# Kernel optimization log

Hardware: AMD Instinct MI355X
Metric: run time of the kernel (lower is better)

Reference implementation:

```python
import jax, jax.numpy as jnp
import numpy as np

EPS = 1e-5

def _bn(x, p):
    # p: (4, C) rows = gamma, beta, running_mean, running_var ; x: (B, C, H, W)
    g, b, m, v = p[0], p[1], p[2], p[3]
    sh = (1, -1, 1, 1)
    return (x - m.reshape(sh)) * (g.reshape(sh) * jax.lax.rsqrt(v.reshape(sh) + EPS)) + b.reshape(sh)

def _cba1(x, w, p):
    # 1x1 conv (no bias) + BN + ReLU
    return jax.nn.relu(_bn(jnp.einsum('oc,bchw->bohw', w, x), p))

def setup_inputs() -> dict:
    B, C, H, W = 2, 512, 128, 256
    CK, K, CO = 256, 19, 512
    key = jax.random.key(0)
    ks = jax.random.split(key, 10)
    def w(k, shape, fan):
        return jax.random.normal(k, shape, jnp.float32) * (fan ** -0.5)
    def bn(c):
        return jnp.stack([jnp.ones((c,), jnp.float32), jnp.zeros((c,), jnp.float32),
                          jnp.zeros((c,), jnp.float32), jnp.ones((c,), jnp.float32)])
    return {
        'x': jax.random.normal(ks[0], (B, C, H, W), jnp.float32),
        'proxy_feats': jax.random.normal(ks[1], (B, C, K, 1), jnp.float32),
        'wq1': w(ks[2], (CK, C), C),  'bnq1': bn(CK),
        'wq2': w(ks[3], (CK, CK), CK), 'bnq2': bn(CK),
        'wk1': w(ks[4], (CK, C), C),  'bnk1': bn(CK),
        'wk2': w(ks[5], (CK, CK), CK), 'bnk2': bn(CK),
        'wv':  w(ks[6], (CK, C), C),  'bnv':  bn(CK),
        'wout': w(ks[7], (C, CK), CK), 'bnout': bn(C),
        'wbot': w(ks[8], (CO, 2 * C, 3, 3), 2 * C * 9), 'bnbot': bn(CO),
    }

def reference(x, proxy_feats, wq1, wq2, wk1, wk2, wv, wout, wbot,
              bnq1, bnq2, bnk1, bnk2, bnv, bnout, bnbot):
    B, C, H, W = x.shape
    CK = wq1.shape[0]
    # --- ObjectContextBlock: pixel-region cross attention ---
    q = _cba1(_cba1(x, wq1, bnq1), wq2, bnq2)            # (B, CK, H, W)
    k = _cba1(_cba1(proxy_feats, wk1, bnk1), wk2, bnk2)  # (B, CK, K, 1)
    v = _cba1(proxy_feats, wv, bnv)                      # (B, CK, K, 1)
    q = q.reshape(B, CK, H * W)                          # (B, CK, N)
    k = k.reshape(B, CK, -1)                             # (B, CK, K)
    v = v.reshape(B, CK, -1)                             # (B, CK, K)
    sim = jnp.einsum('bcn,bck->bnk', q, k) * (CK ** -0.5)
    sim = jax.nn.softmax(sim, axis=-1)                   # (B, N, K)
    ctx = jnp.einsum('bnk,bck->bcn', sim, v).reshape(B, CK, H, W)
    ctx = _cba1(ctx, wout, bnout)                        # (B, C, H, W)
    # --- bottleneck: concat + 3x3 conv + BN + ReLU ---
    cat = jnp.concatenate([ctx, x], axis=1)              # (B, 2C, H, W)
    out = jax.lax.conv_general_dilated(cat, wbot, (1, 1), 'SAME',
                                       dimension_numbers=('NCHW', 'OIHW', 'NCHW'))
    return jax.nn.relu(_bn(out, bnbot))
```

## Files before the change

### kernel.cpp

```cpp
#include <hip/hip_runtime.h>
#include <cstdint>

#define EPS 1e-5f
#define PADW 258
#define PADROWS 33540
#define NPIX 32768

typedef __attribute__((ext_vector_type(8))) short bf16x8;
typedef __attribute__((ext_vector_type(4))) float f32x4;

__device__ __forceinline__ ushort f2bf(float f) {
  union { float f; uint32_t u; } v; v.f = f;
  uint32_t r = v.u + 0x7fffu + ((v.u >> 16) & 1u);
  return (ushort)(r >> 16);
}
__device__ __forceinline__ float bf2f(ushort h) {
  union { uint32_t u; float f; } v; v.u = ((uint32_t)h) << 16;
  return v.f;
}
__device__ __forceinline__ void gload_lds16(const void* g, void* lds) {
  __builtin_amdgcn_global_load_lds((__attribute__((address_space(1))) void*)g,
                                   (__attribute__((address_space(3))) void*)lds,
                                   16, 0, 0);
}

template <int BMODE, int OMODE>
__global__ __launch_bounds__(256) void mfma_gemm(
    const ushort* __restrict__ A, const ushort* __restrict__ B,
    const float* __restrict__ bn, void* __restrict__ OutV,
    int M, int K, int pitchB, int ciB, long strideB, int pitchO, long strideO) {
  const int lane = threadIdx.x & 63;
  const int wave = threadIdx.x >> 6;
  const int wm = (wave & 1) * 64;
  const int wn = (wave >> 1) * 64;
  const int m0 = blockIdx.y * 128;
  const int n0 = blockIdx.x * 128;
  const int z  = blockIdx.z;
  B += (size_t)z * strideB;

  const int h = n0 >> 8, w0 = n0 & 255;
  long prowB;
  if (BMODE == 0) prowB = n0;
  else            prowB = (long)(h + 1) * PADW + (w0 + 1);

  __shared__ __align__(16) ushort Asl[4 * 128 * 8];
  __shared__ __align__(16) ushort Bsl[4 * 128 * 8];

  f32x4 acc[4][4];
#pragma unroll
  for (int mt = 0; mt < 4; ++mt)
#pragma unroll
    for (int nt = 0; nt < 4; ++nt) acc[mt][nt] = (f32x4){0.f, 0.f, 0.f, 0.f};

  for (int k0 = 0; k0 < K; k0 += 32) {
#pragma unroll
    for (int i = 0; i < 2; ++i) {
      int c = (wave * 2 + i) * 64 + lane;
      int mm = c >> 2, g = (c & 3) ^ ((mm >> 1) & 3);
      gload_lds16(A + (size_t)(m0 + mm) * K + (k0 + g * 8), Asl + c * 8);
    }
    long rowb; int cib;
    if (BMODE == 2) {
      int tap = k0 >> 10;
      int dy = tap / 3 - 1, dx = tap % 3 - 1;
      rowb = prowB + dy * PADW + dx;
      cib  = k0 & 1023;
    } else {
      rowb = prowB;
      cib  = ciB + k0;
    }
#pragma unroll
    for (int i = 0; i < 2; ++i) {
      int c = (wave * 2 + i) * 64 + lane;
      int nn = c >> 2, g = (c & 3) ^ ((nn >> 1) & 3);
      gload_lds16(B + (size_t)(rowb + nn) * pitchB + cib + g * 8, Bsl + c * 8);
    }
    __syncthreads();
    bf16x8 af[4], bfr[4];
#pragma unroll
    for (int t = 0; t < 4; ++t) {
      int ks = lane >> 4;
      int ma = wm + t * 16 + (lane & 15);
      int nb = wn + t * 16 + (lane & 15);
      af[t]  = *(const bf16x8*)(Asl + (ma * 4 + (ks ^ ((ma >> 1) & 3))) * 8);
      bfr[t] = *(const bf16x8*)(Bsl + (nb * 4 + (ks ^ ((nb >> 1) & 3))) * 8);
    }
#pragma unroll
    for (int mt = 0; mt < 4; ++mt)
#pragma unroll
      for (int nt = 0; nt < 4; ++nt)
        acc[mt][nt] = __builtin_amdgcn_mfma_f32_16x16x32_bf16(af[mt], bfr[nt], acc[mt][nt], 0, 0, 0);
    __syncthreads();
  }

  const int q4 = lane >> 4, col = lane & 15;
  float scv[16], bov[16];
#pragma unroll
  for (int mt = 0; mt < 4; ++mt)
#pragma unroll
    for (int r = 0; r < 4; ++r) {
      int m = m0 + wm + mt * 16 + q4 * 4 + r;
      float s = bn[m] * rsqrtf(bn[3 * M + m] + EPS);
      scv[mt * 4 + r] = s;
      bov[mt * 4 + r] = bn[M + m] - bn[2 * M + m] * s;
    }
  if (OMODE == 2) {
    float* Outf = (float*)OutV + (size_t)z * strideO;
#pragma unroll
    for (int mt = 0; mt < 4; ++mt)
#pragma unroll
      for (int r = 0; r < 4; ++r) {
        int m = m0 + wm + mt * 16 + q4 * 4 + r;
        float* rowp = Outf + (size_t)m * NPIX + n0 + wn;
#pragma unroll
        for (int nt = 0; nt < 4; ++nt)
          rowp[nt * 16 + col] = fmaxf(acc[mt][nt][r] * scv[mt * 4 + r] + bov[mt * 4 + r], 0.f);
      }
  } else {
    ushort* Outh = (ushort*)OutV + (size_t)z * strideO;
    long prowO = (OMODE == 0) ? (long)n0 : ((long)(h + 1) * PADW + (w0 + 1));
#pragma unroll
    for (int nt = 0; nt < 4; ++nt) {
      long row = prowO + wn + nt * 16 + col;
      ushort* p = Outh + (size_t)row * pitchO + m0 + wm;
#pragma unroll
      for (int mt = 0; mt < 4; ++mt) {
        ushort4 pk;
        pk.x = f2bf(fmaxf(acc[mt][nt][0] * scv[mt * 4 + 0] + bov[mt * 4 + 0], 0.f));
        pk.y = f2bf(fmaxf(acc[mt][nt][1] * scv[mt * 4 + 1] + bov[mt * 4 + 1], 0.f));
        pk.z = f2bf(fmaxf(acc[mt][nt][2] * scv[mt * 4 + 2] + bov[mt * 4 + 2], 0.f));
        pk.w = f2bf(fmaxf(acc[mt][nt][3] * scv[mt * 4 + 3] + bov[mt * 4 + 3], 0.f));
        *(ushort4*)(p + mt * 16 + q4 * 4) = pk;
      }
    }
  }
}

#define PXS  130
#define ROWC (PXS * 4)
#define BUFC (3 * ROWC)
__global__ __launch_bounds__(256, 3) void conv3x3_mfma(
    const ushort* __restrict__ W2, const ushort* __restrict__ cat,
    const float* __restrict__ bn, float* __restrict__ out) {
  const int tid  = threadIdx.x;
  const int lane = tid & 63;
  const int wave = tid >> 6;
  const int wm = (wave & 1) * 64;
  const int wn = (wave >> 1) * 64;
  const int m0 = (blockIdx.x & 3) * 128;
  const int n0 = (blockIdx.x >> 2) * 128;
  const int z  = blockIdx.z;
  const int h = n0 >> 8, w0 = n0 & 255;
  const int prow0 = (h + 1) * PADW + (w0 + 1);
  const ushort* Bz = cat + (size_t)z * PADROWS * 1024;

  __shared__ __align__(16) ushort halo[2 * BUFC * 8];

  f32x4 acc[4][4];
#pragma unroll
  for (int mt = 0; mt < 4; ++mt)
#pragma unroll
    for (int nt = 0; nt < 4; ++nt) acc[mt][nt] = (f32x4){0.f, 0.f, 0.f, 0.f};

  int offs[7];
#pragma unroll
  for (int s = 0; s < 7; ++s) {
    int c = s * 256 + tid;
    if (c < BUFC) {
      int o_slot = c & 3;
      int q = c >> 2;
      int p = q % PXS;
      int r = q / PXS;
      int o_g = o_slot ^ ((p >> 1) & 3);
      offs[s] = ((prow0 + (r - 1) * PADW + (p - 1)) << 10) + o_g * 8;
    } else {
      offs[s] = -1;
    }
  }

  auto stage1 = [&](int s, int buf, int ci0n) {
    if (offs[s] >= 0)
      gload_lds16(Bz + (size_t)offs[s] + ci0n,
                  halo + ((size_t)buf * BUFC + s * 256 + wave * 64) * 8);
  };

  const ushort* Alane = W2 + (size_t)(m0 + wm + (lane & 15)) * 32 + (lane >> 4) * 8;

  const int p0  = wn + (lane & 15);
  const int oct = lane >> 4;
  int hoff0[3];
#pragma unroll
  for (int dx = 0; dx < 3; ++dx) {
    int p = p0 + dx;
    hoff0[dx] = (p * 4 + (oct ^ ((p >> 1) & 3))) * 16;
  }

#pragma unroll
  for (int s = 0; s < 7; ++s) stage1(s, 0, 0);
  bf16x8 af[2][4];
#pragma unroll
  for (int t = 0; t < 2; ++t)
#pragma unroll
    for (int mt = 0; mt < 4; ++mt)
      af[t][mt] = *(const bf16x8*)(Alane + (size_t)t * 16384 + mt * 512);
  asm volatile("s_waitcnt vmcnt(8)" ::: "memory");
  __builtin_amdgcn_sched_barrier(0);
  __builtin_amdgcn_s_barrier();

  for (int it = 0; it < 32; ++it) {
    const ushort* Ait = Alane + (size_t)it * (9 * 16384);
    const ushort* An  = Ait + (size_t)(9 * 16384);
    const char* hb0 = (const char*)(halo + (size_t)(it & 1) * BUFC * 8);
    const int nbuf = (it + 1) & 1;
    const int nci  = (it + 1) * 32;
    const bool more = (it < 31);

#pragma unroll
    for (int t = 0; t < 9; ++t) {
      const int r = t / 3, dx = t % 3;
      bf16x8 bfr[4];
#pragma unroll
      for (int nt = 0; nt < 4; ++nt)
        bfr[nt] = *(const bf16x8*)(hb0 + r * (ROWC * 16) + nt * 1024 + hoff0[dx]);
      if (t < 7 && more) stage1(t, nbuf, nci);
      __builtin_amdgcn_s_barrier();
      asm volatile("s_waitcnt lgkmcnt(0)" ::: "memory");
      __builtin_amdgcn_sched_barrier(0);
      __builtin_amdgcn_s_setprio(1);
#pragma unroll
      for (int nt = 0; nt < 4; ++nt)
#pragma unroll
        for (int mt = 0; mt < 4; ++mt)
          acc[mt][nt] = __builtin_amdgcn_mfma_f32_16x16x32_bf16(
              af[t & 1][mt], bfr[nt], acc[mt][nt], 0, 0, 0);
      __builtin_amdgcn_s_setprio(0);
      if (t < 7) {
#pragma unroll
        for (int mt = 0; mt < 4; ++mt)
          af[t & 1][mt] = *(const bf16x8*)(Ait + (size_t)(t + 2) * 16384 + mt * 512);
      } else if (t == 8 && more) {
#pragma unroll
        for (int mt = 0; mt < 4; ++mt)
          af[0][mt] = *(const bf16x8*)(An + mt * 512);
#pragma unroll
        for (int mt = 0; mt < 4; ++mt)
          af[1][mt] = *(const bf16x8*)(An + 16384 + mt * 512);
      }
      if (t == 8) {
        asm volatile("s_waitcnt vmcnt(8)" ::: "memory");
        __builtin_amdgcn_sched_barrier(0);
      }
      __builtin_amdgcn_s_barrier();
    }
  }

  const int q4 = lane >> 4, col = lane & 15;
  float* Outf = out + (size_t)z * 512 * NPIX;
#pragma unroll
  for (int mt = 0; mt < 4; ++mt)
#pragma unroll
    for (int r = 0; r < 4; ++r) {
      int m = m0 + wm + mt * 16 + q4 * 4 + r;
      float s  = bn[m] * rsqrtf(bn[3 * 512 + m] + EPS);
      float bo = bn[512 + m] - bn[2 * 512 + m] * s;
      float* rowp = Outf + (size_t)m * NPIX + n0 + wn;
#pragma unroll
      for (int nt = 0; nt < 4; ++nt)
        rowp[nt * 16 + col] = fmaxf(acc[mt][nt][r] * s + bo, 0.f);
    }
}

__global__ __launch_bounds__(256) void small_gemm_kernel(
    const float* __restrict__ Wm, const float* __restrict__ X,
    const float* __restrict__ bn, float* __restrict__ Y,
    int CO, int CI, int KC) {
  int co = blockIdx.x, b = blockIdx.y;
  int q = threadIdx.x >> 6, kc = threadIdx.x & 63;
  __shared__ float part[3][24];
  const float* Xb = X + (size_t)b * CI * KC;
  const float* Wr = Wm + (size_t)co * CI;
  float acc = 0.f;
  int cq = CI >> 2;
  if (kc < KC) {
    for (int c = q * cq; c < (q + 1) * cq; ++c)
      acc += Wr[c] * Xb[(size_t)c * KC + kc];
  }
  if (q > 0 && kc < KC) part[q - 1][kc] = acc;
  __syncthreads();
  if (q == 0 && kc < KC) {
    acc += part[0][kc] + part[1][kc] + part[2][kc];
    float s  = bn[co] * rsqrtf(bn[3 * CO + co] + EPS);
    float bs = bn[CO + co] - bn[2 * CO + co] * s;
    Y[((size_t)b * CO + co) * KC + kc] = fmaxf(acc * s + bs, 0.f);
  }
}

__global__ __launch_bounds__(256) void attention_kernel(
    const ushort* __restrict__ qT, const float* __restrict__ Kp,
    const float* __restrict__ Vp, ushort* __restrict__ ctxT) {
  int b = blockIdx.y;
  int pix = blockIdx.x * 256 + threadIdx.x;
  __shared__ float ks[256][19], vs[256][19];
  for (int idx = threadIdx.x; idx < 256 * 19; idx += 256) {
    int c = idx / 19, kk = idx % 19;
    ks[c][kk] = Kp[((size_t)b * 256 + c) * 19 + kk];
    vs[c][kk] = Vp[((size_t)b * 256 + c) * 19 + kk];
  }
  __syncthreads();

  const ushort* qrow = qT + ((size_t)b * NPIX + pix) * 256;
  float sim[19];
#pragma unroll
  for (int kk = 0; kk < 19; ++kk) sim[kk] = 0.f;
  for (int c0 = 0; c0 < 256; c0 += 8) {
    uint4 raw = *(const uint4*)(qrow + c0);
    float qf[8] = {bf2f((ushort)(raw.x & 0xffff)), bf2f((ushort)(raw.x >> 16)),
                   bf2f((ushort)(raw.y & 0xffff)), bf2f((ushort)(raw.y >> 16)),
                   bf2f((ushort)(raw.z & 0xffff)), bf2f((ushort)(raw.z >> 16)),
                   bf2f((ushort)(raw.w & 0xffff)), bf2f((ushort)(raw.w >> 16))};
#pragma unroll
    for (int j = 0; j < 8; ++j)
#pragma unroll
      for (int kk = 0; kk < 19; ++kk) sim[kk] += qf[j] * ks[c0 + j][kk];
  }
  const float scale = 0.0625f;
  float mx = -1e30f;
#pragma unroll
  for (int kk = 0; kk < 19; ++kk) { sim[kk] *= scale; mx = fmaxf(mx, sim[kk]); }
  float denom = 0.f;
#pragma unroll
  for (int kk = 0; kk < 19; ++kk) { sim[kk] = __expf(sim[kk] - mx); denom += sim[kk]; }
  float inv = 1.f / denom;
#pragma unroll
  for (int kk = 0; kk < 19; ++kk) sim[kk] *= inv;

  ushort* crow = ctxT + ((size_t)b * NPIX + pix) * 256;
  for (int c0 = 0; c0 < 256; c0 += 8) {
    uint32_t o[4];
#pragma unroll
    for (int j = 0; j < 4; ++j) {
      float v0 = 0.f, v1 = 0.f;
#pragma unroll
      for (int kk = 0; kk < 19; ++kk) {
        v0 += sim[kk] * vs[c0 + j * 2][kk];
        v1 += sim[kk] * vs[c0 + j * 2 + 1][kk];
      }
      o[j] = (uint32_t)f2bf(v0) | ((uint32_t)f2bf(v1) << 16);
    }
    *(uint4*)(crow + c0) = make_uint4(o[0], o[1], o[2], o[3]);
  }
}

__global__ __launch_bounds__(256) void transpose_x_kernel(
    const float* __restrict__ x, ushort* __restrict__ cat) {
  int b = blockIdx.z, ci0 = blockIdx.y * 64, n0 = blockIdx.x * 64;
  __shared__ float t[64][65];
  const float* xb = x + ((size_t)b * 512 + ci0) * NPIX + n0;
  for (int i = 0; i < 16; ++i) {
    int idx = i * 256 + threadIdx.x;
    int c = idx >> 6, w = idx & 63;
    t[c][w] = xb[(size_t)c * NPIX + w];
  }
  __syncthreads();
  int h = n0 >> 8, w0 = n0 & 255;
  size_t pbase = ((size_t)b * PADROWS + (size_t)(h + 1) * PADW + (w0 + 1)) * 1024 + 512 + ci0;
  for (int i = 0; i < 16; ++i) {
    int idx = i * 256 + threadIdx.x;
    int n = idx >> 6, c = idx & 63;
    cat[pbase + (size_t)n * 1024 + c] = f2bf(t[c][n]);
  }
}

__global__ __launch_bounds__(256) void zero_border_kernel(ushort* __restrict__ cat) {
  int b = blockIdx.y, i = blockIdx.x;
  int row, col;
  if (i < 258)      { row = 0;            col = i; }
  else if (i < 516) { row = 129;          col = i - 258; }
  else if (i < 644) { row = i - 516 + 1;  col = 0; }
  else              { row = i - 644 + 1;  col = 257; }
  size_t base = ((size_t)b * PADROWS + (size_t)row * PADW + col) * 1024 +
                (size_t)threadIdx.x * 4;
  *(ushort4*)(cat + base) = make_ushort4(0, 0, 0, 0);
}

__global__ void convert_w_kernel(const float* __restrict__ in, ushort* __restrict__ out, int n) {
  int i = blockIdx.x * 256 + threadIdx.x;
  if (i < n) out[i] = f2bf(in[i]);
}
__global__ void repack_conv_w_kernel(const float* __restrict__ wbot, ushort* __restrict__ Wrb) {
  int idx = blockIdx.x * 256 + threadIdx.x;
  if (idx >= 512 * 9216) return;
  int ci_in = idx & 31;
  int r  = idx >> 5;
  int co = r & 511;
  int tt = r >> 9;
  int t = tt % 9, chunk = tt / 9;
  Wrb[idx] = f2bf(wbot[((size_t)co * 1024 + chunk * 32 + ci_in) * 9 + t]);
}

extern "C" void kernel_launch(void* const* d_in, const int* in_sizes, int n_in,
                              void* d_out, int out_size, void* d_ws, size_t ws_size,
                              hipStream_t stream) {
  const float* x     = (const float*)d_in[0];
  const float* proxy = (const float*)d_in[1];
  const float* wq1   = (const float*)d_in[2];
  const float* bnq1  = (const float*)d_in[3];
  const float* wq2   = (const float*)d_in[4];
  const float* bnq2  = (const float*)d_in[5];
  const float* wk1   = (const float*)d_in[6];
  const float* bnk1  = (const float*)d_in[7];
  const float* wk2   = (const float*)d_in[8];
  const float* bnk2  = (const float*)d_in[9];
  const float* wv    = (const float*)d_in[10];
  const float* bnv   = (const float*)d_in[11];
  const float* wout  = (const float*)d_in[12];
  const float* bnout = (const float*)d_in[13];
  const float* wbot  = (const float*)d_in[14];
  const float* bnbot = (const float*)d_in[15];
  float* out = (float*)d_out;

  const int B = 2, C = 512, CK = 256, KC = 19;
  char* ws = (char*)d_ws;
  ushort* cat  = (ushort*)ws;
  ushort* bufA = (ushort*)(ws + 137379840);
  ushort* bufB = (ushort*)(ws + 137379840 + 33554432);
  ushort* Wrb  = (ushort*)(ws + 204488704);
  ushort* wq1b = (ushort*)(ws + 213925888);
  ushort* wq2b = (ushort*)(ws + 214188032);
  ushort* woutb= (ushort*)(ws + 214319104);
  float*  k1   = (float*)(ws + 214581248);
  float*  k2   = k1 + (size_t)B * CK * KC;
  float*  vv   = k2 + (size_t)B * CK * KC;

  zero_border_kernel<<<dim3(772, B), 256, 0, stream>>>(cat);

  convert_w_kernel<<<(CK * C + 255) / 256, 256, 0, stream>>>(wq1, wq1b, CK * C);
  convert_w_kernel<<<(CK * CK + 255) / 256, 256, 0, stream>>>(wq2, wq2b, CK * CK);
  convert_w_kernel<<<(C * CK + 255) / 256, 256, 0, stream>>>(wout, woutb, C * CK);
  repack_conv_w_kernel<<<(512 * 9216 + 255) / 256, 256, 0, stream>>>(wbot, Wrb);

  small_gemm_kernel<<<dim3(CK, B), 256, 0, stream>>>(wk1, proxy, bnk1, k1, CK, C, KC);
  small_gemm_kernel<<<dim3(CK, B), 256, 0, stream>>>(wk2, k1, bnk2, k2, CK, CK, KC);
  small_gemm_kernel<<<dim3(CK, B), 256, 0, stream>>>(wv, proxy, bnv, vv, CK, C, KC);

  transpose_x_kernel<<<dim3(NPIX / 64, 8, B), 256, 0, stream>>>(x, cat);

  const long padStride = (long)PADROWS * 1024;
  const long nckStride = (long)NPIX * 256;

  mfma_gemm<1, 0><<<dim3(NPIX / 128, 2, B), 256, 0, stream>>>(
      wq1b, cat, bnq1, bufA, 256, 512, 1024, 512, padStride, 256, nckStride);
  mfma_gemm<0, 0><<<dim3(NPIX / 128, 2, B), 256, 0, stream>>>(
      wq2b, bufA, bnq2, bufB, 256, 256, 256, 0, nckStride, 256, nckStride);

  attention_kernel<<<dim3(NPIX / 256, B), 256, 0, stream>>>(bufB, k2, vv, bufA);

  mfma_gemm<0, 1><<<dim3(NPIX / 128, 4, B), 256, 0, stream>>>(
      woutb, bufA, bnout, cat, 512, 256, 256, 0, nckStride, 1024, padStride);

  conv3x3_mfma<<<dim3((NPIX / 128) * 4, 1, B), 256, 0, stream>>>(Wrb, cat, bnbot, out);
}
```

Measured before the change: 1.105 ms.

## Enlarge conv3x3 tile to 256x256 with 512-thread blocks over full rows

The 3x3 conv kernel now processes a 256-output-channel by full-image-row (256 pixel) tile per block using 8 waves, each computing 64x128 outputs. The halo buffer covers a whole padded row plus borders, so each staged input pixel and each weight fragment are reused across more MFMAs, cutting global/LDS traffic per FLOP. In exchange, accumulator registers double (128 floats per lane), occupancy drops to 2 blocks per CU, and there are fewer blocks (512) to spread across the CUs.

```diff
diff --git a/kernel.cpp b/kernel.cpp
--- a/kernel.cpp
+++ b/kernel.cpp
@@ -136,57 +136,52 @@
   }
 }
 
-#define PXS  130
-#define ROWC (PXS * 4)
-#define BUFC (3 * ROWC)
-__global__ __launch_bounds__(256, 3) void conv3x3_mfma(
+#define PXS2  258
+#define ROWC2 (PXS2 * 4)
+#define BUFC2 (3 * ROWC2)
+#define SLOTS2 3584
+__global__ __launch_bounds__(512, 2) void conv3x3_mfma(
     const ushort* __restrict__ W2, const ushort* __restrict__ cat,
     const float* __restrict__ bn, float* __restrict__ out) {
   const int tid  = threadIdx.x;
   const int lane = tid & 63;
   const int wave = tid >> 6;
-  const int wm = (wave & 1) * 64;
-  const int wn = (wave >> 1) * 64;
-  const int m0 = (blockIdx.x & 3) * 128;
-  const int n0 = (blockIdx.x >> 2) * 128;
+  const int wm  = (wave & 3) * 64;
+  const int wnp = (wave >> 2) * 128;
+  const int m0 = (blockIdx.x & 1) * 256;
+  const int h  = blockIdx.x >> 1;
   const int z  = blockIdx.z;
-  const int h = n0 >> 8, w0 = n0 & 255;
-  const int prow0 = (h + 1) * PADW + (w0 + 1);
   const ushort* Bz = cat + (size_t)z * PADROWS * 1024;
 
-  __shared__ __align__(16) ushort halo[2 * BUFC * 8];
-
-  f32x4 acc[4][4];
+  __shared__ __align__(16) ushort halo[2 * SLOTS2 * 8];
+
+  f32x4 acc[4][8];
 #pragma unroll
   for (int mt = 0; mt < 4; ++mt)
 #pragma unroll
-    for (int nt = 0; nt < 4; ++nt) acc[mt][nt] = (f32x4){0.f, 0.f, 0.f, 0.f};
+    for (int nt = 0; nt < 8; ++nt) acc[mt][nt] = (f32x4){0.f, 0.f, 0.f, 0.f};
 
   int offs[7];
 #pragma unroll
   for (int s = 0; s < 7; ++s) {
-    int c = s * 256 + tid;
-    if (c < BUFC) {
-      int o_slot = c & 3;
-      int q = c >> 2;
-      int p = q % PXS;
-      int r = q / PXS;
-      int o_g = o_slot ^ ((p >> 1) & 3);
-      offs[s] = ((prow0 + (r - 1) * PADW + (p - 1)) << 10) + o_g * 8;
-    } else {
-      offs[s] = -1;
-    }
+    int c = s * 512 + tid;
+    if (c > BUFC2 - 1) c = BUFC2 - 1;
+    int o_slot = c & 3;
+    int q = c >> 2;
+    int p = q % PXS2;
+    int r = q / PXS2;
+    int o_g = o_slot ^ ((p >> 1) & 3);
+    offs[s] = (((h + r) * PADW + p) << 10) + o_g * 8;
   }
 
   auto stage1 = [&](int s, int buf, int ci0n) {
-    if (offs[s] >= 0)
-      gload_lds16(Bz + (size_t)offs[s] + ci0n,
-                  halo + ((size_t)buf * BUFC + s * 256 + wave * 64) * 8);
+    gload_lds16(Bz + (size_t)offs[s] + ci0n,
+                halo + ((size_t)buf * SLOTS2 + s * 512 + wave * 64) * 8);
   };
 
   const ushort* Alane = W2 + (size_t)(m0 + wm + (lane & 15)) * 32 + (lane >> 4) * 8;
 
-  const int p0  = wn + (lane & 15);
+  const int p0  = wnp + (lane & 15);
   const int oct = lane >> 4;
   int hoff0[3];
 #pragma unroll
@@ -210,7 +205,7 @@
   for (int it = 0; it < 32; ++it) {
     const ushort* Ait = Alane + (size_t)it * (9 * 16384);
     const ushort* An  = Ait + (size_t)(9 * 16384);
-    const char* hb0 = (const char*)(halo + (size_t)(it & 1) * BUFC * 8);
+    const char* hb0 = (const char*)(halo + (size_t)(it & 1) * SLOTS2 * 8);
     const int nbuf = (it + 1) & 1;
     const int nci  = (it + 1) * 32;
     const bool more = (it < 31);
@@ -218,17 +213,17 @@
 #pragma unroll
     for (int t = 0; t < 9; ++t) {
       const int r = t / 3, dx = t % 3;
-      bf16x8 bfr[4];
-#pragma unroll
-      for (int nt = 0; nt < 4; ++nt)
-        bfr[nt] = *(const bf16x8*)(hb0 + r * (ROWC * 16) + nt * 1024 + hoff0[dx]);
+      bf16x8 bfr[8];
+#pragma unroll
+      for (int nt = 0; nt < 8; ++nt)
+        bfr[nt] = *(const bf16x8*)(hb0 + r * (ROWC2 * 16) + nt * 1024 + hoff0[dx]);
       if (t < 7 && more) stage1(t, nbuf, nci);
       __builtin_amdgcn_s_barrier();
       asm volatile("s_waitcnt lgkmcnt(0)" ::: "memory");
       __builtin_amdgcn_sched_barrier(0);
       __builtin_amdgcn_s_setprio(1);
 #pragma unroll
-      for (int nt = 0; nt < 4; ++nt)
+      for (int nt = 0; nt < 8; ++nt)
 #pragma unroll
         for (int mt = 0; mt < 4; ++mt)
           acc[mt][nt] = __builtin_amdgcn_mfma_f32_16x16x32_bf16(
@@ -263,9 +258,9 @@
       int m = m0 + wm + mt * 16 + q4 * 4 + r;
       float s  = bn[m] * rsqrtf(bn[3 * 512 + m] + EPS);
       float bo = bn[512 + m] - bn[2 * 512 + m] * s;
-      float* rowp = Outf + (size_t)m * NPIX + n0 + wn;
-#pragma unroll
-      for (int nt = 0; nt < 4; ++nt)
+      float* rowp = Outf + (size_t)m * NPIX + h * 256 + wnp;
+#pragma unroll
+      for (int nt = 0; nt < 8; ++nt)
         rowp[nt * 16 + col] = fmaxf(acc[mt][nt][r] * s + bo, 0.f);
     }
 }
@@ -458,5 +453,5 @@
   mfma_gemm<0, 1><<<dim3(NPIX / 128, 4, B), 256, 0, stream>>>(
       woutb, bufA, bnout, cat, 512, 256, 256, 0, nckStride, 1024, padStride);
 
-  conv3x3_mfma<<<dim3((NPIX / 128) * 4, 1, B), 256, 0, stream>>>(Wrb, cat, bnbot, out);
-}
+  conv3x3_mfma<<<dim3(256, 1, B), 512, 0, stream>>>(Wrb, cat, bnbot, out);
+}
```

Measured after the change: 1.045 ms. -5.4%, faster.
